# Kernel optimization log

Hardware: AMD Instinct MI355X
Metric: run time of the kernel (lower is better)

Reference implementation:

```python
import jax, jax.numpy as jnp
import numpy as np

DIM = 192
HEADS = 4
EPS_LN = 1e-5
EPS_NORM = 1e-12


def _layernorm(x, w, b):
    # x: [b, c, h, w]; normalize over channel dim (equiv to 'b (h w) c' LN over last axis)
    mu = jnp.mean(x, axis=1, keepdims=True)
    var = jnp.mean((x - mu) ** 2, axis=1, keepdims=True)
    return (x - mu) / jnp.sqrt(var + EPS_LN) * w[None, :, None, None] + b[None, :, None, None]


def _conv1x1(x, w):
    # w: [out_c, in_c]
    return jnp.einsum('bchw,oc->bohw', x, w)


def _dwconv3x3(x, w):
    # w: [c, 1, 3, 3], depthwise (groups = c), padding 1
    return jax.lax.conv_general_dilated(
        x, w, window_strides=(1, 1), padding='SAME',
        feature_group_count=x.shape[1],
        dimension_numbers=('NCHW', 'OIHW', 'NCHW'))


def _l2norm(x):
    # F.normalize(dim=-1): x / max(||x||_2, eps)
    n = jnp.sqrt(jnp.sum(x * x, axis=-1, keepdims=True))
    return x / jnp.maximum(n, EPS_NORM)


def setup_inputs() -> dict:
    key = jax.random.key(0)
    ks = jax.random.split(key, 10)
    b, c, h, w = 8, DIM, 128, 128
    inp = {
        'xx': jax.random.normal(ks[0], (b, c, h, w), jnp.float32),
        'q_in': jax.random.normal(ks[1], (b, c, h, w), jnp.float32),
        'ln_w': jnp.ones((c,), jnp.float32),
        'ln_b': jnp.zeros((c,), jnp.float32),
        'w_q': jax.random.normal(ks[2], (c, c), jnp.float32) * 0.02,
        'w_k': jax.random.normal(ks[3], (c, c), jnp.float32) * 0.02,
        'w_v': jax.random.normal(ks[4], (c, c), jnp.float32) * 0.02,
        'wd_q': jax.random.normal(ks[5], (c, 1, 3, 3), jnp.float32) * 0.1,
        'wd_k': jax.random.normal(ks[6], (c, 1, 3, 3), jnp.float32) * 0.1,
        'wd_v': jax.random.normal(ks[7], (c, 1, 3, 3), jnp.float32) * 0.1,
        'w_proj': jax.random.normal(ks[8], (c, c), jnp.float32) * 0.02,
        'temperature': jnp.ones((HEADS, 1, 1), jnp.float32),
    }
    return inp


def reference(xx, q_in, ln_w, ln_b, w_q, w_k, w_v, wd_q, wd_k, wd_v, w_proj, temperature):
    b, c, h, w = xx.shape
    hw = h * w
    dh = c // HEADS  # per-head channel dim

    x_n = _layernorm(xx, ln_w, ln_b)
    q_n = _layernorm(q_in, ln_w, ln_b)

    q = _dwconv3x3(_conv1x1(q_n, w_q), wd_q)
    k = _dwconv3x3(_conv1x1(x_n, w_k), wd_k)
    v = _dwconv3x3(_conv1x1(x_n, w_v), wd_v)

    # b (head c) h w -> b head c (h w)
    q = q.reshape(b, HEADS, dh, hw)
    k = k.reshape(b, HEADS, dh, hw)
    v = v.reshape(b, HEADS, dh, hw)

    q = _l2norm(q)
    k = _l2norm(k)

    # channel-channel attention: [b, head, dh, dh]
    attn = jnp.einsum('bhcn,bhdn->bhcd', q, k) * temperature[None]
    attn = jax.nn.softmax(attn, axis=-1)

    out = jnp.einsum('bhcd,bhdn->bhcn', attn, v)  # [b, head, dh, hw]
    out = out.reshape(b, c, h, w)
    out = _conv1x1(out, w_proj) + q_in
    return out
```

## Files before the change

### kernel.cpp

```cpp
#include <hip/hip_runtime.h>
#include <hip/hip_bf16.h>
#include <stdint.h>

#define HWSZ 16384
#define CCH 192
#define NB 8
#define NHEAD 4
#define DHEAD 48

typedef unsigned short u16;
typedef __bf16 bf16x8 __attribute__((ext_vector_type(8)));
typedef float f32x4 __attribute__((ext_vector_type(4)));
typedef short s16x8 __attribute__((ext_vector_type(8)));
typedef short s16x4 __attribute__((ext_vector_type(4)));

__device__ __forceinline__ float b2f(u16 h){
  union { unsigned u; float f; } v; v.u = ((unsigned)h) << 16; return v.f;
}
__device__ __forceinline__ u16 f2b(float f){
  union { float f; unsigned u; } v; v.f = f;
  unsigned r = v.u + 0x7fffu + ((v.u >> 16) & 1u);
  return (u16)(r >> 16);
}

__global__ __launch_bounds__(256) void k_wpack(
    const float* __restrict__ wq, const float* __restrict__ wk,
    const float* __restrict__ wv,
    const float* __restrict__ lnw, const float* __restrict__ lnb,
    u16* __restrict__ o, float* __restrict__ ad)
{
  int m = blockIdx.x;
  const float* src = (m == 0) ? wq : (m == 1) ? wk : wv;
  u16* dst = o + (size_t)m * CCH * CCH;
  int t = threadIdx.x;
  if (t < CCH){
    const float* row = src + (size_t)t * CCH;
    float a = 0.f, d = 0.f;
    for (int c = 0; c < CCH; c += 4){
      float4 w = *(const float4*)(row + c);
      float4 g = *(const float4*)(lnw + c);
      float4 bb = *(const float4*)(lnb + c);
      u16 p0 = f2b(w.x * g.x), p1 = f2b(w.y * g.y);
      u16 p2 = f2b(w.z * g.z), p3 = f2b(w.w * g.w);
      a += b2f(p0) + b2f(p1) + b2f(p2) + b2f(p3);
      d += w.x * bb.x + w.y * bb.y + w.z * bb.z + w.w * bb.w;
      s16x4 pk;
      pk[0] = (short)p0; pk[1] = (short)p1; pk[2] = (short)p2; pk[3] = (short)p3;
      *(s16x4*)(dst + (size_t)t * CCH + c) = pk;
    }
    ad[(m * 2 + 0) * CCH + t] = a;
    ad[(m * 2 + 1) * CCH + t] = d;
  }
}

__global__ __launch_bounds__(512, 2) void k_convf2(
    const float* __restrict__ xx, const float* __restrict__ q_in,
    const u16* __restrict__ Wb, const float* __restrict__ ad,
    u16* __restrict__ Ok, u16* __restrict__ Ov, u16* __restrict__ Oq)
{
  __shared__ u16 lnT[6 * 16 * 2 * 264];
  __shared__ float2 redf[8][256];
  __shared__ float mu_s[256];
  __shared__ float rs_s[256];
  int tid = threadIdx.x;
  int b = blockIdx.y, z = blockIdx.z;
  int p0 = blockIdx.x * 256;
  int lane = tid & 63, w = tid >> 6;
  int grp = tid & 31;
  int cr  = tid >> 5;

  const float* xb = (z ? q_in : xx) + (size_t)b * CCH * HWSZ + p0 + grp * 8;

  float s[8] = {}, ss[8] = {};
  #pragma unroll
  for (int pass = 0; pass < 2; ++pass){
    float4 v[12];
    #pragma unroll
    for (int ii = 0; ii < 6; ++ii){
      int c = (pass * 6 + ii) * 16 + cr;
      v[2*ii]   = *(const float4*)(xb + (size_t)c * HWSZ);
      v[2*ii+1] = *(const float4*)(xb + (size_t)c * HWSZ + 4);
    }
    #pragma unroll
    for (int ii = 0; ii < 6; ++ii){
      int c = (pass * 6 + ii) * 16 + cr;
      float e0 = v[2*ii].x,   e1 = v[2*ii].y,   e2 = v[2*ii].z,   e3 = v[2*ii].w;
      float e4 = v[2*ii+1].x, e5 = v[2*ii+1].y, e6 = v[2*ii+1].z, e7 = v[2*ii+1].w;
      s[0]+=e0; ss[0]+=e0*e0; s[1]+=e1; ss[1]+=e1*e1;
      s[2]+=e2; ss[2]+=e2*e2; s[3]+=e3; ss[3]+=e3*e3;
      s[4]+=e4; ss[4]+=e4*e4; s[5]+=e5; ss[5]+=e5*e5;
      s[6]+=e6; ss[6]+=e6*e6; s[7]+=e7; ss[7]+=e7*e7;
      s16x8 pk;
      pk[0]=(short)f2b(e0); pk[1]=(short)f2b(e1); pk[2]=(short)f2b(e2); pk[3]=(short)f2b(e3);
      pk[4]=(short)f2b(e4); pk[5]=(short)f2b(e5); pk[6]=(short)f2b(e6); pk[7]=(short)f2b(e7);
      int kb = c >> 5, kr = c & 31;
      int tile = (kr >> 2) & 1;
      int mr   = ((kr >> 3) << 2) | (kr & 3);
      int ti   = (kb * 16 + (grp >> 1)) * 2 + tile;
      *(s16x8*)(&lnT[ti * 264 + mr * 16 + (grp & 1) * 8]) = pk;
    }
  }
  #pragma unroll
  for (int j = 0; j < 8; ++j){
    s[j]  += __shfl_xor(s[j],  32);
    ss[j] += __shfl_xor(ss[j], 32);
  }
  if (lane < 32){
    #pragma unroll
    for (int j = 0; j < 8; ++j)
      redf[w][grp * 8 + j] = make_float2(s[j], ss[j]);
  }
  __syncthreads();
  if (tid < 256){
    float sa = 0.f, qa = 0.f;
    #pragma unroll
    for (int ww = 0; ww < 8; ++ww){
      float2 t = redf[ww][tid];
      sa += t.x; qa += t.y;
    }
    float mu = sa * (1.f / CCH);
    float var = qa * (1.f / CCH) - mu * mu;
    mu_s[tid] = mu;
    rs_s[tid] = rsqrtf(var + 1e-5f);
  }
  __syncthreads();

  int quad = lane >> 4, r = lane & 15;
  int wm = (w & 3) * 48;
  int mi, nh0, nhn;
  if (z == 0){ mi = (w >> 2) + 1; nh0 = 0; nhn = 4; }
  else       { mi = 0; nh0 = (w >> 2) * 2; nhn = 2; }
  const u16* A0 = Wb + (size_t)mi * CCH * CCH + (size_t)wm * CCH;
  const float* aA = ad + (mi * 2 + 0) * CCH;
  const float* dA = ad + (mi * 2 + 1) * CCH;
  u16* O = z ? Oq : ((w >> 2) ? Ov : Ok);
  size_t ob = (size_t)b * CCH * HWSZ;
  unsigned lvb0 = (unsigned)(uintptr_t)(&lnT[0]) + 2u * (unsigned)(r + quad * 64);

  float a_o[3], d_o[3];
  #pragma unroll
  for (int i = 0; i < 3; ++i){
    a_o[i] = aA[wm + i * 16 + r];
    d_o[i] = dA[wm + i * 16 + r];
  }

  for (int hh = 0; hh < nhn; ++hh){
    int nh = nh0 + hh;
    f32x4 acc[3][4] = {};
    bf16x8 aC[3], aN[3];
    #pragma unroll
    for (int i = 0; i < 3; ++i)
      aC[i] = *(const bf16x8*)(A0 + (size_t)(i * 16 + r) * CCH + quad * 8);
    #pragma unroll
    for (int kb = 0; kb < 6; ++kb){
      s16x4 lo[4], hi[4];
      #pragma unroll
      for (int j = 0; j < 4; ++j){
        unsigned a = lvb0 + (unsigned)(kb * 16896 + (nh * 4 + j) * 1056);
        asm volatile("ds_read_b64_tr_b16 %0, %1" : "=&v"(lo[j]) : "v"(a));
        asm volatile("ds_read_b64_tr_b16 %0, %1 offset:528" : "=&v"(hi[j]) : "v"(a));
      }
      if (kb < 5){
        #pragma unroll
        for (int i = 0; i < 3; ++i)
          aN[i] = *(const bf16x8*)(A0 + (size_t)(i * 16 + r) * CCH + (kb + 1) * 32 + quad * 8);
      }
      asm volatile("s_waitcnt lgkmcnt(0)" ::: "memory");
      __builtin_amdgcn_sched_barrier(0);
      #pragma unroll
      for (int j = 0; j < 4; ++j){
        union { s16x8 s; bf16x8 b; } u;
        u.s = __builtin_shufflevector(lo[j], hi[j], 0, 1, 2, 3, 4, 5, 6, 7);
        #pragma unroll
        for (int i = 0; i < 3; ++i)
          acc[i][j] = __builtin_amdgcn_mfma_f32_16x16x32_bf16(u.b, aC[i], acc[i][j], 0, 0, 0);
      }
      #pragma unroll
      for (int i = 0; i < 3; ++i) aC[i] = aN[i];
    }
    #pragma unroll
    for (int j = 0; j < 4; ++j){
      int pxb = nh * 64 + j * 16 + quad * 4;
      f32x4 mu4 = *(const f32x4*)(&mu_s[pxb]);
      f32x4 rs4 = *(const f32x4*)(&rs_s[pxb]);
      #pragma unroll
      for (int i = 0; i < 3; ++i){
        s16x4 pk;
        #pragma unroll
        for (int rg = 0; rg < 4; ++rg){
          float val = rs4[rg] * (acc[i][j][rg] - mu4[rg] * a_o[i]) + d_o[i];
          pk[rg] = (short)f2b(val);
        }
        int o = wm + i * 16 + r;
        *(s16x4*)(&O[ob + (size_t)o * HWSZ + p0 + pxb]) = pk;
      }
    }
  }
}

__global__ __launch_bounds__(256) void k_dw3(
    const float* __restrict__ wq, const float* __restrict__ wk,
    const float* __restrict__ wv,
    u16* __restrict__ bq, u16* __restrict__ bk, u16* __restrict__ bv,
    float* __restrict__ ssq_q, float* __restrict__ ssq_k)
{
  int tid = threadIdx.x;
  int bc  = blockIdx.x;
  int z   = blockIdx.y;
  int c   = bc % CCH;
  const float* wd = (z == 0) ? wq : (z == 1) ? wk : wv;
  u16* buf = (z == 0) ? bq : (z == 1) ? bk : bv;
  float w[9];
  #pragma unroll
  for (int t = 0; t < 9; ++t) w[t] = wd[c * 9 + t];
  u16* p = buf + (size_t)bc * HWSZ;

  int xseg = tid & 15, ygrp = tid >> 4;
  int x0 = xseg * 8, y0 = ygrp * 8;

  s16x8 zz = {0,0,0,0,0,0,0,0};
  s16x8 raw[10];
  #pragma unroll
  for (int rr = 0; rr < 10; ++rr){
    int yy = y0 - 1 + rr;
    raw[rr] = (yy >= 0 && yy < 128) ? *(const s16x8*)(p + yy * 128 + x0) : zz;
  }
  __syncthreads();

  float cf[10][8];
  float lf[10], rgt[10];
  #pragma unroll
  for (int rr = 0; rr < 10; ++rr){
    #pragma unroll
    for (int j = 0; j < 8; ++j) cf[rr][j] = b2f((u16)raw[rr][j]);
    float l  = __shfl_up(cf[rr][7], 1);
    float rr_ = __shfl_down(cf[rr][0], 1);
    lf[rr]  = (xseg > 0)  ? l   : 0.f;
    rgt[rr] = (xseg < 15) ? rr_ : 0.f;
  }

  float ss = 0.f;
  #pragma unroll
  for (int k = 0; k < 8; ++k){
    float acc[8] = {0.f,0.f,0.f,0.f,0.f,0.f,0.f,0.f};
    #pragma unroll
    for (int dy = 0; dy < 3; ++dy){
      int rr = k + dy;
      float wl = w[dy * 3], wc = w[dy * 3 + 1], wr = w[dy * 3 + 2];
      acc[0] += wl * lf[rr] + wc * cf[rr][0] + wr * cf[rr][1];
      #pragma unroll
      for (int j = 1; j < 7; ++j)
        acc[j] += wl * cf[rr][j - 1] + wc * cf[rr][j] + wr * cf[rr][j + 1];
      acc[7] += wl * cf[rr][6] + wc * cf[rr][7] + wr * rgt[rr];
    }
    s16x8 pk;
    #pragma unroll
    for (int j = 0; j < 8; ++j){
      pk[j] = (short)f2b(acc[j]);
      ss += acc[j] * acc[j];
    }
    *(s16x8*)(p + (y0 + k) * 128 + x0) = pk;
  }

  if (z < 2){
    #pragma unroll
    for (int m = 32; m > 0; m >>= 1) ss += __shfl_xor(ss, m);
    if ((tid & 63) == 0) atomicAdd(&((z == 0) ? ssq_q : ssq_k)[bc], ss);
  }
}

__global__ void k_gram(const u16* __restrict__ q, const u16* __restrict__ k,
                       float* __restrict__ G)
{
  __shared__ float gs[4 * 48 * 49];
  int tid = threadIdx.x;
  int chunk = blockIdx.x;
  int h = blockIdx.y, b = blockIdx.z;
  int lane = tid & 63, w = tid >> 6;
  int quad = lane >> 4, r = lane & 15;
  int nb = chunk * 1024 + w * 256;
  const u16* qb = q + ((size_t)b * CCH + h * DHEAD) * HWSZ;
  const u16* kb = k + ((size_t)b * CCH + h * DHEAD) * HWSZ;
  f32x4 acc[3][3] = {};
  for (int s = 0; s < 8; ++s){
    int kk = nb + s * 32 + quad * 8;
    bf16x8 af[3], bfr[3];
    #pragma unroll
    for (int i = 0; i < 3; ++i){
      af[i]  = *(const bf16x8*)(qb + (size_t)(i * 16 + r) * HWSZ + kk);
      bfr[i] = *(const bf16x8*)(kb + (size_t)(i * 16 + r) * HWSZ + kk);
    }
    #pragma unroll
    for (int i = 0; i < 3; ++i)
      #pragma unroll
      for (int j = 0; j < 3; ++j)
        acc[i][j] = __builtin_amdgcn_mfma_f32_16x16x32_bf16(af[i], bfr[j], acc[i][j], 0, 0, 0);
  }
  float* gw = gs + w * (48 * 49);
  #pragma unroll
  for (int i = 0; i < 3; ++i)
    #pragma unroll
    for (int j = 0; j < 3; ++j)
      #pragma unroll
      for (int rg = 0; rg < 4; ++rg){
        int row = i * 16 + quad * 4 + rg;
        int col = j * 16 + r;
        gw[row * 49 + col] = acc[i][j][rg];
      }
  __syncthreads();
  float* gb = G + (size_t)(b * NHEAD + h) * (DHEAD * DHEAD);
  #pragma unroll
  for (int t = 0; t < 9; ++t){
    int e = t * 256 + tid;
    int row = e / 48, col = e - row * 48;
    int o = row * 49 + col;
    float s = gs[o] + gs[48 * 49 + o] + gs[2 * 48 * 49 + o] + gs[3 * 48 * 49 + o];
    atomicAdd(&gb[e], s);
  }
}

__global__ __launch_bounds__(256) void k_mk(
    const float* __restrict__ G, const float* __restrict__ ssq_q,
    const float* __restrict__ ssq_k, const float* __restrict__ temp,
    const float* __restrict__ wp, u16* __restrict__ Mout)
{
  __shared__ u16 Pt[48 * 72];
  __shared__ u16 wA[192 * 72];
  __shared__ float rks[48];
  int tid = threadIdx.x;
  int h = blockIdx.x, b = blockIdx.y;
  {
    s16x8 z = {};
    #pragma unroll
    for (int i = 0; i < 2; ++i){
      int idx = (i * 256 + tid) * 8;
      if (idx < 48 * 72) *(s16x8*)(&Pt[idx]) = z;
    }
    #pragma unroll
    for (int i = 0; i < 7; ++i){
      int idx = (i * 256 + tid) * 8;
      if (idx < 192 * 72) *(s16x8*)(&wA[idx]) = z;
    }
  }
  if (tid < DHEAD)
    rks[tid] = 1.f / fmaxf(sqrtf(ssq_k[b * CCH + h * DHEAD + tid]), 1e-12f);
  __syncthreads();
  if (tid < DHEAD){
    float rq = temp[h] / fmaxf(sqrtf(ssq_q[b * CCH + h * DHEAD + tid]), 1e-12f);
    const float* gr = G + (size_t)(b * NHEAD + h) * (DHEAD * DHEAD) + tid * DHEAD;
    float a[DHEAD];
    float mx = -1e30f;
    #pragma unroll
    for (int d = 0; d < DHEAD; ++d){
      a[d] = gr[d] * rq * rks[d];
      mx = fmaxf(mx, a[d]);
    }
    float sum = 0.f;
    #pragma unroll
    for (int d = 0; d < DHEAD; ++d){ a[d] = __expf(a[d] - mx); sum += a[d]; }
    float inv = 1.f / sum;
    #pragma unroll
    for (int d = 0; d < DHEAD; ++d) Pt[d * 72 + tid] = f2b(a[d] * inv);
  }
  {
    const float* wb = wp + h * DHEAD;
    #pragma unroll
    for (int i = 0; i < 9; ++i){
      int e = (i * 256 + tid) * 4;
      int row = e / DHEAD, col = e - row * DHEAD;
      float4 v = *(const float4*)(wb + (size_t)row * CCH + col);
      s16x4 pk;
      pk[0] = (short)f2b(v.x); pk[1] = (short)f2b(v.y);
      pk[2] = (short)f2b(v.z); pk[3] = (short)f2b(v.w);
      *(s16x4*)(&wA[row * 72 + col]) = pk;
    }
  }
  __syncthreads();
  int lane = tid & 63, wid = tid >> 6;
  int quad = lane >> 4, r = lane & 15;
  int wm = wid * 48;
  f32x4 acc[3][3] = {};
  #pragma unroll
  for (int ks = 0; ks < 2; ++ks){
    int k0 = ks * 32;
    bf16x8 af[3], bf[3];
    #pragma unroll
    for (int i = 0; i < 3; ++i)
      af[i] = *(const bf16x8*)(&wA[(wm + i * 16 + r) * 72 + k0 + quad * 8]);
    #pragma unroll
    for (int j = 0; j < 3; ++j)
      bf[j] = *(const bf16x8*)(&Pt[(j * 16 + r) * 72 + k0 + quad * 8]);
    #pragma unroll
    for (int i = 0; i < 3; ++i)
      #pragma unroll
      for (int j = 0; j < 3; ++j)
        acc[i][j] = __builtin_amdgcn_mfma_f32_16x16x32_bf16(af[i], bf[j], acc[i][j], 0, 0, 0);
  }
  u16* mb = Mout + (size_t)b * (CCH * CCH) + h * DHEAD;
  #pragma unroll
  for (int i = 0; i < 3; ++i)
    #pragma unroll
    for (int j = 0; j < 3; ++j)
      #pragma unroll
      for (int rg = 0; rg < 4; ++rg){
        int o = wm + i * 16 + quad * 4 + rg;
        int d = j * 16 + r;
        mb[(size_t)o * CCH + d] = f2b(acc[i][j][rg]);
      }
}

__global__ __launch_bounds__(256) void k_gemmv(
    const u16* __restrict__ M, const u16* __restrict__ V,
    float* __restrict__ Out, const float* __restrict__ resid)
{
  __shared__ u16 lA[64 * 200];
  __shared__ u16 lV[96 * 264];
  int tid = threadIdx.x;
  int n0 = blockIdx.x * 128;
  int m0 = blockIdx.y * 64;
  int b  = blockIdx.z;
  {
    const u16* ap = M + (size_t)b * (CCH * CCH) + m0 * CCH;
    #pragma unroll
    for (int i = 0; i < 6; ++i){
      int off = (i * 256 + tid) * 8;
      int row = off / CCH, col = off - row * CCH;
      *(int4*)(&lA[row * 200 + col]) = *(const int4*)(ap + off);
    }
  }
  {
    const u16* vp = V + (size_t)b * CCH * HWSZ + n0;
    #pragma unroll
    for (int i = 0; i < 12; ++i){
      int e = i * 256 + tid;
      int c = e >> 4, ns = (e & 15) * 8;
      int4 v = *(const int4*)(vp + (size_t)c * HWSZ + ns);
      int kb = c >> 5, kr = c & 31;
      int tile = (kr >> 2) & 1;
      int mr = ((kr >> 3) << 2) | (kr & 3);
      int ti = (kb * 8 + (ns >> 4)) * 2 + tile;
      *(int4*)(&lV[ti * 264 + mr * 16 + (ns & 15)]) = v;
    }
  }
  __syncthreads();
  int lane = tid & 63, wid = tid >> 6;
  int quad = lane >> 4, r = lane & 15;
  int wm = (wid >> 1) * 32, wn = (wid & 1) * 64;
  unsigned lvb = (unsigned)(uintptr_t)(&lV[0]) + 2u * (unsigned)(r + quad * 64)
               + (unsigned)((wn >> 4) * 2) * 528u;
  f32x4 acc[2][4] = {};
  #pragma unroll
  for (int kb = 0; kb < 6; ++kb){
    int k0 = kb * 32;
    s16x4 lo[4], hi[4];
    #pragma unroll
    for (int j = 0; j < 4; ++j){
      unsigned a = lvb + (unsigned)kb * 8448u + (unsigned)j * 1056u;
      asm volatile("ds_read_b64_tr_b16 %0, %1" : "=&v"(lo[j]) : "v"(a));
      asm volatile("ds_read_b64_tr_b16 %0, %1 offset:528" : "=&v"(hi[j]) : "v"(a));
    }
    bf16x8 af[2];
    #pragma unroll
    for (int i = 0; i < 2; ++i)
      af[i] = *(const bf16x8*)(&lA[(wm + i * 16 + r) * 200 + k0 + quad * 8]);
    asm volatile("s_waitcnt lgkmcnt(0)" ::: "memory");
    __builtin_amdgcn_sched_barrier(0);
    #pragma unroll
    for (int j = 0; j < 4; ++j){
      union { s16x8 s; bf16x8 b; } u;
      u.s = __builtin_shufflevector(lo[j], hi[j], 0, 1, 2, 3, 4, 5, 6, 7);
      #pragma unroll
      for (int i = 0; i < 2; ++i)
        acc[i][j] = __builtin_amdgcn_mfma_f32_16x16x32_bf16(af[i], u.b, acc[i][j], 0, 0, 0);
    }
  }
  size_t obase = (size_t)b * CCH * HWSZ;
  #pragma unroll
  for (int i = 0; i < 2; ++i){
    #pragma unroll
    for (int rg = 0; rg < 4; ++rg){
      int o = m0 + wm + i * 16 + quad * 4 + rg;
      size_t rowb = obase + (size_t)o * HWSZ;
      #pragma unroll
      for (int j = 0; j < 4; ++j){
        int n = n0 + wn + j * 16 + r;
        Out[rowb + n] = acc[i][j][rg] + resid[rowb + n];
      }
    }
  }
}

extern "C" void kernel_launch(void* const* d_in, const int* in_sizes, int n_in,
                              void* d_out, int out_size, void* d_ws, size_t ws_size,
                              hipStream_t stream)
{
  const float* xx     = (const float*)d_in[0];
  const float* q_in   = (const float*)d_in[1];
  const float* ln_w   = (const float*)d_in[2];
  const float* ln_b   = (const float*)d_in[3];
  const float* w_q    = (const float*)d_in[4];
  const float* w_k    = (const float*)d_in[5];
  const float* w_v    = (const float*)d_in[6];
  const float* wd_q   = (const float*)d_in[7];
  const float* wd_k   = (const float*)d_in[8];
  const float* wd_v   = (const float*)d_in[9];
  const float* w_proj = (const float*)d_in[10];
  const float* temp   = (const float*)d_in[11];

  const size_t SZ = (size_t)NB * CCH * HWSZ;
  u16* B1 = (u16*)d_ws;
  u16* B2 = B1 + SZ;
  u16* B3 = B2 + SZ;
  float* G     = (float*)(B3 + SZ);
  float* ssq_q = G + 32 * DHEAD * DHEAD;
  float* ssq_k = ssq_q + NB * CCH;
  u16* Mb      = (u16*)(ssq_k + NB * CCH);
  u16* Wb      = Mb + (size_t)NB * CCH * CCH;
  float* Ad    = (float*)(Wb + 3 * CCH * CCH);

  hipMemsetAsync(G, 0, (size_t)(32 * DHEAD * DHEAD + 2 * NB * CCH) * sizeof(float), stream);

  k_wpack<<<3, 256, 0, stream>>>(w_q, w_k, w_v, ln_w, ln_b, Wb, Ad);
  k_convf2<<<dim3(64, NB, 2), 512, 0, stream>>>(
      xx, q_in, Wb, Ad, B2, B1, B3);
  k_dw3<<<dim3(NB * CCH, 3), 256, 0, stream>>>(wd_q, wd_k, wd_v,
                                               B3, B2, B1, ssq_q, ssq_k);
  k_gram<<<dim3(16, NHEAD, NB), 256, 0, stream>>>(B3, B2, G);
  k_mk<<<dim3(NHEAD, NB), 256, 0, stream>>>(G, ssq_q, ssq_k, temp, w_proj, Mb);
  k_gemmv<<<dim3(128, 3, NB), 256, 0, stream>>>(Mb, B1, (float*)d_out, q_in);
}
```

Baseline: 445.7 us.

## Pipeline LayerNorm input staging with first-head MFMA in the fused conv kernel

The fused LayerNorm+1x1-conv kernel now streams the input channels in 32-channel chunks with a three-deep register buffer. It runs the first head's MFMA k-block as soon as each chunk reaches LDS, with a barrier per chunk, instead of staging all 192 channels before any matrix work. The goal is to overlap global load latency with tensor-core compute. The launch-bounds minimum-blocks hint of 2 is also dropped, which loosens register limits but may lower occupancy and adds six block barriers.

Measured after the change: 491.1 us. 10.2% more time.

```diff
diff --git a/kernel.cpp b/kernel.cpp
--- a/kernel.cpp
+++ b/kernel.cpp
@@ -53,7 +53,7 @@
   }
 }
 
-__global__ __launch_bounds__(512, 2) void k_convf2(
+__global__ __launch_bounds__(512) void k_convf3(
     const float* __restrict__ xx, const float* __restrict__ q_in,
     const u16* __restrict__ Wb, const float* __restrict__ ad,
     u16* __restrict__ Ok, u16* __restrict__ Ov, u16* __restrict__ Oq)
@@ -70,60 +70,6 @@
   int cr  = tid >> 5;
 
   const float* xb = (z ? q_in : xx) + (size_t)b * CCH * HWSZ + p0 + grp * 8;
-
-  float s[8] = {}, ss[8] = {};
-  #pragma unroll
-  for (int pass = 0; pass < 2; ++pass){
-    float4 v[12];
-    #pragma unroll
-    for (int ii = 0; ii < 6; ++ii){
-      int c = (pass * 6 + ii) * 16 + cr;
-      v[2*ii]   = *(const float4*)(xb + (size_t)c * HWSZ);
-      v[2*ii+1] = *(const float4*)(xb + (size_t)c * HWSZ + 4);
-    }
-    #pragma unroll
-    for (int ii = 0; ii < 6; ++ii){
-      int c = (pass * 6 + ii) * 16 + cr;
-      float e0 = v[2*ii].x,   e1 = v[2*ii].y,   e2 = v[2*ii].z,   e3 = v[2*ii].w;
-      float e4 = v[2*ii+1].x, e5 = v[2*ii+1].y, e6 = v[2*ii+1].z, e7 = v[2*ii+1].w;
-      s[0]+=e0; ss[0]+=e0*e0; s[1]+=e1; ss[1]+=e1*e1;
-      s[2]+=e2; ss[2]+=e2*e2; s[3]+=e3; ss[3]+=e3*e3;
-      s[4]+=e4; ss[4]+=e4*e4; s[5]+=e5; ss[5]+=e5*e5;
-      s[6]+=e6; ss[6]+=e6*e6; s[7]+=e7; ss[7]+=e7*e7;
-      s16x8 pk;
-      pk[0]=(short)f2b(e0); pk[1]=(short)f2b(e1); pk[2]=(short)f2b(e2); pk[3]=(short)f2b(e3);
-      pk[4]=(short)f2b(e4); pk[5]=(short)f2b(e5); pk[6]=(short)f2b(e6); pk[7]=(short)f2b(e7);
-      int kb = c >> 5, kr = c & 31;
-      int tile = (kr >> 2) & 1;
-      int mr   = ((kr >> 3) << 2) | (kr & 3);
-      int ti   = (kb * 16 + (grp >> 1)) * 2 + tile;
-      *(s16x8*)(&lnT[ti * 264 + mr * 16 + (grp & 1) * 8]) = pk;
-    }
-  }
-  #pragma unroll
-  for (int j = 0; j < 8; ++j){
-    s[j]  += __shfl_xor(s[j],  32);
-    ss[j] += __shfl_xor(ss[j], 32);
-  }
-  if (lane < 32){
-    #pragma unroll
-    for (int j = 0; j < 8; ++j)
-      redf[w][grp * 8 + j] = make_float2(s[j], ss[j]);
-  }
-  __syncthreads();
-  if (tid < 256){
-    float sa = 0.f, qa = 0.f;
-    #pragma unroll
-    for (int ww = 0; ww < 8; ++ww){
-      float2 t = redf[ww][tid];
-      sa += t.x; qa += t.y;
-    }
-    float mu = sa * (1.f / CCH);
-    float var = qa * (1.f / CCH) - mu * mu;
-    mu_s[tid] = mu;
-    rs_s[tid] = rsqrtf(var + 1e-5f);
-  }
-  __syncthreads();
 
   int quad = lane >> 4, r = lane & 15;
   int wm = (w & 3) * 48;
@@ -144,19 +90,103 @@
     d_o[i] = dA[wm + i * 16 + r];
   }
 
-  for (int hh = 0; hh < nhn; ++hh){
-    int nh = nh0 + hh;
-    f32x4 acc[3][4] = {};
-    bf16x8 aC[3], aN[3];
-    #pragma unroll
-    for (int i = 0; i < 3; ++i)
-      aC[i] = *(const bf16x8*)(A0 + (size_t)(i * 16 + r) * CCH + quad * 8);
-    #pragma unroll
-    for (int kb = 0; kb < 6; ++kb){
+  auto epilogue = [&](int nh, f32x4 (&ac)[3][4]){
+    #pragma unroll
+    for (int j = 0; j < 4; ++j){
+      int pxb = nh * 64 + j * 16 + quad * 4;
+      f32x4 mu4 = *(const f32x4*)(&mu_s[pxb]);
+      f32x4 rs4 = *(const f32x4*)(&rs_s[pxb]);
+      #pragma unroll
+      for (int i = 0; i < 3; ++i){
+        s16x4 pk;
+        #pragma unroll
+        for (int rg = 0; rg < 4; ++rg){
+          float val = rs4[rg] * (ac[i][j][rg] - mu4[rg] * a_o[i]) + d_o[i];
+          pk[rg] = (short)f2b(val);
+        }
+        int o = wm + i * 16 + r;
+        *(s16x4*)(&O[ob + (size_t)o * HWSZ + p0 + pxb]) = pk;
+      }
+    }
+  };
+
+  float s[8] = {}, ss[8] = {};
+  float4 vb[3][4];
+  #pragma unroll
+  for (int t = 0; t < 2; ++t){
+    vb[0][2*t]   = *(const float4*)(xb + (size_t)(t * 16 + cr) * HWSZ);
+    vb[0][2*t+1] = *(const float4*)(xb + (size_t)(t * 16 + cr) * HWSZ + 4);
+  }
+  #pragma unroll
+  for (int t = 0; t < 2; ++t){
+    vb[1][2*t]   = *(const float4*)(xb + (size_t)(32 + t * 16 + cr) * HWSZ);
+    vb[1][2*t+1] = *(const float4*)(xb + (size_t)(32 + t * 16 + cr) * HWSZ + 4);
+  }
+
+  f32x4 acc[3][4] = {};
+  bf16x8 aC[3], aN[3];
+  #pragma unroll
+  for (int i = 0; i < 3; ++i)
+    aC[i] = *(const bf16x8*)(A0 + (size_t)(i * 16 + r) * CCH + quad * 8);
+
+  #pragma unroll
+  for (int kb = 0; kb < 6; ++kb){
+    if (kb < 4){
+      #pragma unroll
+      for (int t = 0; t < 2; ++t){
+        vb[(kb + 2) % 3][2*t]   = *(const float4*)(xb + (size_t)((kb + 2) * 32 + t * 16 + cr) * HWSZ);
+        vb[(kb + 2) % 3][2*t+1] = *(const float4*)(xb + (size_t)((kb + 2) * 32 + t * 16 + cr) * HWSZ + 4);
+      }
+    }
+    #pragma unroll
+    for (int t = 0; t < 2; ++t){
+      float4 v0 = vb[kb % 3][2*t], v1 = vb[kb % 3][2*t+1];
+      float e0 = v0.x, e1 = v0.y, e2 = v0.z, e3 = v0.w;
+      float e4 = v1.x, e5 = v1.y, e6 = v1.z, e7 = v1.w;
+      s[0]+=e0; ss[0]+=e0*e0; s[1]+=e1; ss[1]+=e1*e1;
+      s[2]+=e2; ss[2]+=e2*e2; s[3]+=e3; ss[3]+=e3*e3;
+      s[4]+=e4; ss[4]+=e4*e4; s[5]+=e5; ss[5]+=e5*e5;
+      s[6]+=e6; ss[6]+=e6*e6; s[7]+=e7; ss[7]+=e7*e7;
+      s16x8 pk;
+      pk[0]=(short)f2b(e0); pk[1]=(short)f2b(e1); pk[2]=(short)f2b(e2); pk[3]=(short)f2b(e3);
+      pk[4]=(short)f2b(e4); pk[5]=(short)f2b(e5); pk[6]=(short)f2b(e6); pk[7]=(short)f2b(e7);
+      int kr = t * 16 + cr;
+      int tile = (kr >> 2) & 1;
+      int mr   = ((kr >> 3) << 2) | (kr & 3);
+      int ti   = (kb * 16 + (grp >> 1)) * 2 + tile;
+      *(s16x8*)(&lnT[ti * 264 + mr * 16 + (grp & 1) * 8]) = pk;
+    }
+    if (kb == 5){
+      #pragma unroll
+      for (int j = 0; j < 8; ++j){
+        s[j]  += __shfl_xor(s[j],  32);
+        ss[j] += __shfl_xor(ss[j], 32);
+      }
+      if (lane < 32){
+        #pragma unroll
+        for (int j = 0; j < 8; ++j)
+          redf[w][grp * 8 + j] = make_float2(s[j], ss[j]);
+      }
+    }
+    asm volatile("s_waitcnt lgkmcnt(0)" ::: "memory");
+    __builtin_amdgcn_s_barrier();
+    if (kb == 5 && tid < 256){
+      float sa = 0.f, qa = 0.f;
+      #pragma unroll
+      for (int ww = 0; ww < 8; ++ww){
+        float2 t2 = redf[ww][tid];
+        sa += t2.x; qa += t2.y;
+      }
+      float mu = sa * (1.f / CCH);
+      float var = qa * (1.f / CCH) - mu * mu;
+      mu_s[tid] = mu;
+      rs_s[tid] = rsqrtf(var + 1e-5f);
+    }
+    {
       s16x4 lo[4], hi[4];
       #pragma unroll
       for (int j = 0; j < 4; ++j){
-        unsigned a = lvb0 + (unsigned)(kb * 16896 + (nh * 4 + j) * 1056);
+        unsigned a = lvb0 + (unsigned)(kb * 16896 + (nh0 * 4 + j) * 1056);
         asm volatile("ds_read_b64_tr_b16 %0, %1" : "=&v"(lo[j]) : "v"(a));
         asm volatile("ds_read_b64_tr_b16 %0, %1 offset:528" : "=&v"(hi[j]) : "v"(a));
       }
@@ -178,23 +208,46 @@
       #pragma unroll
       for (int i = 0; i < 3; ++i) aC[i] = aN[i];
     }
-    #pragma unroll
-    for (int j = 0; j < 4; ++j){
-      int pxb = nh * 64 + j * 16 + quad * 4;
-      f32x4 mu4 = *(const f32x4*)(&mu_s[pxb]);
-      f32x4 rs4 = *(const f32x4*)(&rs_s[pxb]);
-      #pragma unroll
-      for (int i = 0; i < 3; ++i){
-        s16x4 pk;
+  }
+  asm volatile("s_waitcnt lgkmcnt(0)" ::: "memory");
+  __builtin_amdgcn_s_barrier();
+  epilogue(nh0, acc);
+
+  for (int hh = 1; hh < nhn; ++hh){
+    int nh = nh0 + hh;
+    f32x4 acc2[3][4] = {};
+    bf16x8 bC[3], bN[3];
+    #pragma unroll
+    for (int i = 0; i < 3; ++i)
+      bC[i] = *(const bf16x8*)(A0 + (size_t)(i * 16 + r) * CCH + quad * 8);
+    #pragma unroll
+    for (int kb = 0; kb < 6; ++kb){
+      s16x4 lo[4], hi[4];
+      #pragma unroll
+      for (int j = 0; j < 4; ++j){
+        unsigned a = lvb0 + (unsigned)(kb * 16896 + (nh * 4 + j) * 1056);
+        asm volatile("ds_read_b64_tr_b16 %0, %1" : "=&v"(lo[j]) : "v"(a));
+        asm volatile("ds_read_b64_tr_b16 %0, %1 offset:528" : "=&v"(hi[j]) : "v"(a));
+      }
+      if (kb < 5){
         #pragma unroll
-        for (int rg = 0; rg < 4; ++rg){
-          float val = rs4[rg] * (acc[i][j][rg] - mu4[rg] * a_o[i]) + d_o[i];
-          pk[rg] = (short)f2b(val);
-        }
-        int o = wm + i * 16 + r;
-        *(s16x4*)(&O[ob + (size_t)o * HWSZ + p0 + pxb]) = pk;
-      }
-    }
+        for (int i = 0; i < 3; ++i)
+          bN[i] = *(const bf16x8*)(A0 + (size_t)(i * 16 + r) * CCH + (kb + 1) * 32 + quad * 8);
+      }
+      asm volatile("s_waitcnt lgkmcnt(0)" ::: "memory");
+      __builtin_amdgcn_sched_barrier(0);
+      #pragma unroll
+      for (int j = 0; j < 4; ++j){
+        union { s16x8 s; bf16x8 b; } u;
+        u.s = __builtin_shufflevector(lo[j], hi[j], 0, 1, 2, 3, 4, 5, 6, 7);
+        #pragma unroll
+        for (int i = 0; i < 3; ++i)
+          acc2[i][j] = __builtin_amdgcn_mfma_f32_16x16x32_bf16(u.b, bC[i], acc2[i][j], 0, 0, 0);
+      }
+      #pragma unroll
+      for (int i = 0; i < 3; ++i) bC[i] = bN[i];
+    }
+    epilogue(nh, acc2);
   }
 }
 
@@ -521,7 +574,7 @@
   hipMemsetAsync(G, 0, (size_t)(32 * DHEAD * DHEAD + 2 * NB * CCH) * sizeof(float), stream);
 
   k_wpack<<<3, 256, 0, stream>>>(w_q, w_k, w_v, ln_w, ln_b, Wb, Ad);
-  k_convf2<<<dim3(64, NB, 2), 512, 0, stream>>>(
+  k_convf3<<<dim3(64, NB, 2), 512, 0, stream>>>(
       xx, q_in, Wb, Ad, B2, B1, B3);
   k_dw3<<<dim3(NB * CCH, 3), 256, 0, stream>>>(wd_q, wd_k, wd_v,
                                                B3, B2, B1, ssq_q, ssq_k);
```
